# Performance work log

Hardware: AMD Instinct MI355X
Metric: run time of the kernel (lower is better)

## Reference

```python
import jax, jax.numpy as jnp
import numpy as np

B, N, C, H = 2, 2048, 1024, 16
D = C // H  # head_dim = 64


def setup_inputs() -> dict:
    key = jax.random.key(0)
    k1, k2, k3, k4 = jax.random.split(key, 4)
    x = jax.random.normal(k1, (B, N, C), dtype=jnp.float32)
    # params (torch Linear: y = x @ W.T + b). Store as [in, out] for einsum.
    w_qkv = jax.random.normal(k2, (C, 3 * C), dtype=jnp.float32) * (1.0 / np.sqrt(C))
    w_out = jax.random.normal(k3, (C, C), dtype=jnp.float32) * (1.0 / np.sqrt(C))
    b_out = jax.random.normal(k4, (C,), dtype=jnp.float32) * 0.01
    # causal mask: 1 above the diagonal -> masked_fill(-inf)
    attn_mask = jnp.triu(jnp.ones((N, N), dtype=jnp.int32), k=1)
    return {"x": x, "w_qkv": w_qkv, "w_out": w_out, "b_out": b_out, "attn_mask": attn_mask}


def reference(x, w_qkv, w_out, b_out, attn_mask):
    b, n, c = x.shape
    scale = 1.0 / jnp.sqrt(jnp.asarray(D, dtype=x.dtype))
    qkv = jnp.einsum('bnc,cd->bnd', x, w_qkv)                # [B, N, 3C]
    qkv = qkv.reshape(b, n, 3, H, D)
    q = qkv[:, :, 0].transpose(0, 2, 1, 3)                   # [B, H, N, D]
    k = qkv[:, :, 1].transpose(0, 2, 1, 3)
    v = qkv[:, :, 2].transpose(0, 2, 1, 3)
    scores = jnp.einsum('bhqd,bhkd->bhqk', q, k) * scale     # [B, H, N, N]
    scores = jnp.where(attn_mask == 1, jnp.asarray(-jnp.inf, dtype=scores.dtype), scores)
    attn = jax.nn.softmax(scores, axis=-1)
    # dropout is identity in eval mode (deterministic reference)
    out = jnp.einsum('bhqk,bhkd->bhqd', attn, v)             # [B, H, N, D]
    out = out.transpose(0, 2, 1, 3).reshape(b, n, c)         # [B, N, C]
    return jnp.einsum('bnc,cd->bnd', out, w_out) + b_out
```

## Files before the change

### kernel.cpp

```cpp
#include <hip/hip_runtime.h>

typedef _Float16 f16;
typedef _Float16 f16x8 __attribute__((ext_vector_type(8)));
typedef _Float16 f16x4 __attribute__((ext_vector_type(4)));
typedef float    f32x4 __attribute__((ext_vector_type(4)));

#define MFMA16(a, b, c) __builtin_amdgcn_mfma_f32_16x16x32_f16((a), (b), (c), 0, 0, 0)

__device__ __forceinline__ void gload16(const void* g, void* l) {
  __builtin_amdgcn_global_load_lds(
      (const __attribute__((address_space(1))) unsigned int*)g,
      (__attribute__((address_space(3))) unsigned int*)l, 16, 0, 0);
}

__device__ __forceinline__ float ex2(float x) {
  float r;
  asm("v_exp_f32 %0, %1" : "=v"(r) : "v"(x));
  return r;
}


__global__ void cast_f32_f16(const float* __restrict__ in, f16* __restrict__ out, int n4) {
  int i = blockIdx.x * blockDim.x + threadIdx.x;
  if (i < n4) {
    float4 v = ((const float4*)in)[i];
    f16x4 o;
    o.x = (f16)v.x; o.y = (f16)v.y; o.z = (f16)v.z; o.w = (f16)v.w;
    ((f16x4*)out)[i] = o;
  }
}

__global__ void transpose_cast(const float* __restrict__ in, f16* __restrict__ out, int R, int Cc) {
  __shared__ float tile[32][33];
  int c0 = blockIdx.x * 32, r0 = blockIdx.y * 32;
  int tx = threadIdx.x, ty = threadIdx.y;
#pragma unroll
  for (int i = ty; i < 32; i += 8)
    tile[i][tx] = in[(size_t)(r0 + i) * Cc + c0 + tx];
  __syncthreads();
#pragma unroll
  for (int i = ty; i < 32; i += 8)
    out[(size_t)(c0 + i) * R + r0 + tx] = (f16)tile[tx][i];
}

template <int KDIM>
__device__ __forceinline__ void gemm_core(const f16* __restrict__ A, const f16* __restrict__ Bt,
                                          int bm, int bn, f16* lA, f16* lB, f32x4 acc[4][4]) {
  const int t = threadIdx.x, lane = t & 63, wave = t >> 6;
  const int wm = wave >> 1, wn = wave & 1;
  const int srow = lane >> 3;
  const int skb = (lane & 7) * 16;
  const int nkt = KDIM / 64;
  for (int kt = 0; kt < nkt; ++kt) {
    __syncthreads();
#pragma unroll
    for (int c = 0; c < 4; ++c) {
      int cc = c * 4 + wave;
      int row = cc * 8 + srow;
      int kbs = skb ^ ((row & 7) << 4);
      gload16((const char*)A + (size_t)(bm * 128 + row) * (KDIM * 2) + kt * 128 + kbs,
              lA + cc * 512);
      gload16((const char*)Bt + (size_t)(bn * 128 + row) * (KDIM * 2) + kt * 128 + kbs,
              lB + cc * 512);
    }
    __syncthreads();
#pragma unroll
    for (int ks = 0; ks < 2; ++ks) {
      f16x8 af[4], bf[4];
#pragma unroll
      for (int mi = 0; mi < 4; ++mi) {
        int r = wm * 64 + mi * 16 + (lane & 15);
        int ke = (ks * 32 + ((lane >> 4) << 3)) ^ ((r & 7) << 3);
        af[mi] = *(const f16x8*)&lA[r * 64 + ke];
      }
#pragma unroll
      for (int ni = 0; ni < 4; ++ni) {
        int r = wn * 64 + ni * 16 + (lane & 15);
        int ke = (ks * 32 + ((lane >> 4) << 3)) ^ ((r & 7) << 3);
        bf[ni] = *(const f16x8*)&lB[r * 64 + ke];
      }
#pragma unroll
      for (int mi = 0; mi < 4; ++mi)
#pragma unroll
        for (int ni = 0; ni < 4; ++ni)
          acc[mi][ni] = MFMA16(af[mi], bf[ni], acc[mi][ni]);
    }
  }
}

__global__ __launch_bounds__(256, 2) void gemm_qkv(const f16* __restrict__ A,
                                                   const f16* __restrict__ Bt,
                                                   f16* __restrict__ Qo, f16* __restrict__ Ko,
                                                   f16* __restrict__ Vt) {
  __shared__ __align__(16) f16 lA[128 * 64];
  __shared__ __align__(16) f16 lB[128 * 64];
  f32x4 acc[4][4] = {};
  int w = blockIdx.x;
  int xcd = w & 7, i = w >> 3;
  int xr = xcd >> 1, xc = xcd & 1;
  int bm = xr * 8 + (i & 7);
  int bn = xc * 12 + (i >> 3);
  gemm_core<1024>(A, Bt, bm, bn, lA, lB, acc);
  int lane = threadIdx.x & 63, wave = threadIdx.x >> 6;
  int wm = wave >> 1, wn = wave & 1;
  int sec = (bn * 128) >> 10;
  float scl = (sec == 0) ? 0.18033688f : 1.0f;
#pragma unroll
  for (int mi = 0; mi < 4; ++mi)
#pragma unroll
    for (int ni = 0; ni < 4; ++ni)
#pragma unroll
      for (int reg = 0; reg < 4; ++reg) {
        int gr = bm * 128 + wm * 64 + mi * 16 + ((lane >> 4) << 2) + reg;
        int gc = bn * 128 + wn * 64 + ni * 16 + (lane & 15);
        int b = gr >> 11, n = gr & 2047;
        int jj = gc & 1023;
        int h = jj >> 6, d = jj & 63;
        f16 v = (f16)(acc[mi][ni][reg] * scl);
        size_t bh = (size_t)(b * 16 + h);
        if (sec == 0)      Qo[(bh * 2048 + n) * 64 + d] = v;
        else if (sec == 1) Ko[(bh * 2048 + n) * 64 + d] = v;
        else {
          int np = (n & ~31) | (((n >> 2) & 3) << 3) | (((n >> 4) & 1) << 2) | (n & 3);
          Vt[(bh * 64 + d) * 2048 + np] = v;
        }
      }
}

__device__ __forceinline__ void attn_one(const f16* __restrict__ Qb, const f16* __restrict__ Kb,
                                         const f16* __restrict__ Vb, f16* __restrict__ Ob,
                                         int qt, int lane, int wave, f16* lK, f16* lV) {
  const int N = 2048;
  const int wq0 = qt * 64 + wave * 16;
  const int g = lane >> 4, q15 = lane & 15;
  f16x8 qf[2];
#pragma unroll
  for (int ks = 0; ks < 2; ++ks)
    qf[ks] = *(const f16x8*)&Qb[(size_t)(wq0 + q15) * 64 + ks * 32 + (g << 3)];
  f32x4 oacc[4] = {};
  float mrun = -1e30f, lrun = 0.f;
  const int srow = lane >> 3, skb = (lane & 7) * 16;
  const int ntiles = qt + 1;

  auto STAGE = [&](int buf, int kv) {
    int kv0 = kv << 6;
#pragma unroll
    for (int c = 0; c < 2; ++c) {
      int cc = c * 4 + wave;
      int row = cc * 8 + srow;
      int kbs = skb ^ ((row & 7) << 4);
      gload16((const char*)Kb + (size_t)(kv0 + row) * 128 + kbs, lK + buf * 4096 + cc * 512);
      gload16((const char*)Vb + (size_t)row * (N * 2) + (size_t)kv0 * 2 + kbs,
              lV + buf * 4096 + cc * 512);
    }
  };

  STAGE(0, 0);
  __syncthreads();
  for (int kv = 0; kv < ntiles; ++kv) {
    int cur = kv & 1;
    if (kv + 1 < ntiles) STAGE(cur ^ 1, kv + 1);
    const f16* K0 = lK + cur * 4096;
    const f16* V0 = lV + cur * 4096;
    int kv0 = kv << 6;
    f32x4 s[4] = {};
    __builtin_amdgcn_s_setprio(1);
#pragma unroll
    for (int ks = 0; ks < 2; ++ks) {
      f16x8 kf[4];
#pragma unroll
      for (int ni = 0; ni < 4; ++ni) {
        int r = ni * 16 + q15;
        int ke = (ks * 32 + (g << 3)) ^ ((r & 7) << 3);
        kf[ni] = *(const f16x8*)&K0[r * 64 + ke];
      }
#pragma unroll
      for (int ni = 0; ni < 4; ++ni) s[ni] = MFMA16(kf[ni], qf[ks], s[ni]);
    }
    __builtin_amdgcn_s_setprio(0);
    if (kv == qt) {
      int gq = wq0 + q15;
#pragma unroll
      for (int ni = 0; ni < 4; ++ni)
#pragma unroll
        for (int reg = 0; reg < 4; ++reg) {
          int gk = kv0 + ni * 16 + g * 4 + reg;
          if (gk > gq) s[ni][reg] = -1e30f;
        }
    }
    f32x4 m4 = s[0];
#pragma unroll
    for (int ni = 1; ni < 4; ++ni)
#pragma unroll
      for (int reg = 0; reg < 4; ++reg) m4[reg] = fmaxf(m4[reg], s[ni][reg]);
    float mx = fmaxf(fmaxf(m4[0], m4[1]), fmaxf(m4[2], m4[3]));
    mx = fmaxf(mx, __shfl_xor(mx, 16));
    mx = fmaxf(mx, __shfl_xor(mx, 32));
    if (__any(mx > mrun)) {
      float mnew = fmaxf(mrun, mx);
      float corr = ex2(mrun - mnew);
      mrun = mnew;
      lrun *= corr;
#pragma unroll
      for (int ni = 0; ni < 4; ++ni)
#pragma unroll
        for (int reg = 0; reg < 4; ++reg) oacc[ni][reg] *= corr;
    }
    float rsum = 0.f;
#pragma unroll
    for (int ni = 0; ni < 4; ++ni)
#pragma unroll
      for (int reg = 0; reg < 4; ++reg) {
        float p = ex2(s[ni][reg] - mrun);
        s[ni][reg] = p;
        rsum += p;
      }
    rsum += __shfl_xor(rsum, 16);
    rsum += __shfl_xor(rsum, 32);
    lrun += rsum;
    f16x8 pf[2];
#pragma unroll
    for (int ks = 0; ks < 2; ++ks)
#pragma unroll
      for (int e = 0; e < 8; ++e) pf[ks][e] = (f16)s[2 * ks + (e >> 2)][e & 3];
    __builtin_amdgcn_s_setprio(1);
#pragma unroll
    for (int ks = 0; ks < 2; ++ks) {
      f16x8 vf[4];
#pragma unroll
      for (int mi = 0; mi < 4; ++mi) {
        int r = mi * 16 + q15;
        int ke = (ks * 32 + (g << 3)) ^ ((r & 7) << 3);
        vf[mi] = *(const f16x8*)&V0[r * 64 + ke];
      }
#pragma unroll
      for (int mi = 0; mi < 4; ++mi) oacc[mi] = MFMA16(vf[mi], pf[ks], oacc[mi]);
    }
    __builtin_amdgcn_s_setprio(0);
    __syncthreads();
  }
  float inv = 1.0f / lrun;
  int gq = wq0 + q15;
#pragma unroll
  for (int mi = 0; mi < 4; ++mi) {
    f16x4 o4;
#pragma unroll
    for (int reg = 0; reg < 4; ++reg) o4[reg] = (f16)(oacc[mi][reg] * inv);
    *(f16x4*)&Ob[(size_t)gq * 1024 + mi * 16 + g * 4] = o4;
  }
}

__global__ __launch_bounds__(256, 2) void attn(const f16* __restrict__ Q,
                                               const f16* __restrict__ K,
                                               const f16* __restrict__ Vt,
                                               f16* __restrict__ O) {
  __shared__ __align__(16) f16 lK[2 * 4096];
  __shared__ __align__(16) f16 lV[2 * 4096];
  int w = blockIdx.x;
  int c = w & 7, j = w >> 3;
  int bh = c * 4 + (j >> 4);
  int x = j & 15;
  int b = bh >> 4, h = bh & 15;
  int lane = threadIdx.x & 63, wave = threadIdx.x >> 6;
  const f16* Qb = Q + (size_t)bh * 2048 * 64;
  const f16* Kb = K + (size_t)bh * 2048 * 64;
  const f16* Vb = Vt + (size_t)bh * 2048 * 64;
  f16* Ob = O + (size_t)b * 2048 * 1024 + h * 64;
  attn_one(Qb, Kb, Vb, Ob, 31 - x, lane, wave, lK, lV);
  attn_one(Qb, Kb, Vb, Ob, x, lane, wave, lK, lV);
}

__global__ __launch_bounds__(256, 2) void gemm_out(const f16* __restrict__ A,
                                                   const f16* __restrict__ Bt,
                                                   const float* __restrict__ bias,
                                                   float* __restrict__ out) {
  __shared__ __align__(16) f16 lA[128 * 64];
  __shared__ __align__(16) f16 lB[128 * 64];
  f32x4 acc[4][4] = {};
  int w = blockIdx.x;
  int xcd = w & 7, i = w >> 3;
  int bm = xcd * 4 + (i & 3);
  int bn = i >> 2;
  gemm_core<1024>(A, Bt, bm, bn, lA, lB, acc);
  int lane = threadIdx.x & 63, wave = threadIdx.x >> 6;
  int wm = wave >> 1, wn = wave & 1;
#pragma unroll
  for (int mi = 0; mi < 4; ++mi)
#pragma unroll
    for (int ni = 0; ni < 4; ++ni)
#pragma unroll
      for (int reg = 0; reg < 4; ++reg) {
        int gr = bm * 128 + wm * 64 + mi * 16 + ((lane >> 4) << 2) + reg;
        int gc = bn * 128 + wn * 64 + ni * 16 + (lane & 15);
        out[(size_t)gr * 1024 + gc] = acc[mi][ni][reg] + bias[gc];
      }
}

extern "C" void kernel_launch(void* const* d_in, const int* in_sizes, int n_in,
                              void* d_out, int out_size, void* d_ws, size_t ws_size,
                              hipStream_t stream) {
  const float* x     = (const float*)d_in[0];
  const float* w_qkv = (const float*)d_in[1];
  const float* w_out = (const float*)d_in[2];
  const float* b_out = (const float*)d_in[3];
  float* out = (float*)d_out;
  char* ws = (char*)d_ws;

  f16* xh    = (f16*)(ws);
  f16* wqkvT = (f16*)(ws + (8u << 20));
  f16* woutT = (f16*)(ws + (14u << 20));
  f16* Qs    = (f16*)(ws + (16u << 20));
  f16* Ks    = (f16*)(ws + (24u << 20));
  f16* Vts   = (f16*)(ws + (32u << 20));
  f16* Oa    = (f16*)(ws + (40u << 20));

  cast_f32_f16<<<4096, 256, 0, stream>>>(x, xh, 1048576);
  transpose_cast<<<dim3(96, 32), dim3(32, 8), 0, stream>>>(w_qkv, wqkvT, 1024, 3072);
  transpose_cast<<<dim3(32, 32), dim3(32, 8), 0, stream>>>(w_out, woutT, 1024, 1024);
  gemm_qkv<<<768, 256, 0, stream>>>(xh, wqkvT, Qs, Ks, Vts);
  attn<<<512, 256, 0, stream>>>(Qs, Ks, Vts, Oa);
  gemm_out<<<256, 256, 0, stream>>>(Oa, woutT, b_out, out);
}
```

Measured before the change: 118.2 us.

## Double-buffer GEMM LDS tiles and widen attention KV tiles to 128

The shared GEMM core now double-buffers its A/B LDS tiles, so the next k-tile's global-to-LDS load is issued while MFMAs run on the current one. It also raises wave priority around the MFMA block and drops one barrier per iteration. Attention now processes 128 keys per iteration instead of 64, halving the number of loop iterations, barriers and softmax rescale checks, with the causal mask applied on the last tile. The cost is twice the LDS per block in all kernels (64KB each) and more registers for scores in attention, which may lower occupancy. Attention also does more masked wasted work on the diagonal tile.

```diff
diff --git a/kernel.cpp b/kernel.cpp
--- a/kernel.cpp
+++ b/kernel.cpp
@@ -51,19 +51,28 @@
   const int srow = lane >> 3;
   const int skb = (lane & 7) * 16;
   const int nkt = KDIM / 64;
-  for (int kt = 0; kt < nkt; ++kt) {
-    __syncthreads();
+
+  auto STAGE = [&](int buf, int kt) {
 #pragma unroll
     for (int c = 0; c < 4; ++c) {
       int cc = c * 4 + wave;
       int row = cc * 8 + srow;
       int kbs = skb ^ ((row & 7) << 4);
       gload16((const char*)A + (size_t)(bm * 128 + row) * (KDIM * 2) + kt * 128 + kbs,
-              lA + cc * 512);
+              lA + buf * 8192 + cc * 512);
       gload16((const char*)Bt + (size_t)(bn * 128 + row) * (KDIM * 2) + kt * 128 + kbs,
-              lB + cc * 512);
-    }
-    __syncthreads();
+              lB + buf * 8192 + cc * 512);
+    }
+  };
+
+  STAGE(0, 0);
+  __syncthreads();
+  for (int kt = 0; kt < nkt; ++kt) {
+    int cur = kt & 1;
+    if (kt + 1 < nkt) STAGE(cur ^ 1, kt + 1);
+    const f16* A0 = lA + cur * 8192;
+    const f16* B0 = lB + cur * 8192;
+    __builtin_amdgcn_s_setprio(1);
 #pragma unroll
     for (int ks = 0; ks < 2; ++ks) {
       f16x8 af[4], bf[4];
@@ -71,13 +80,13 @@
       for (int mi = 0; mi < 4; ++mi) {
         int r = wm * 64 + mi * 16 + (lane & 15);
         int ke = (ks * 32 + ((lane >> 4) << 3)) ^ ((r & 7) << 3);
-        af[mi] = *(const f16x8*)&lA[r * 64 + ke];
+        af[mi] = *(const f16x8*)&A0[r * 64 + ke];
       }
 #pragma unroll
       for (int ni = 0; ni < 4; ++ni) {
         int r = wn * 64 + ni * 16 + (lane & 15);
         int ke = (ks * 32 + ((lane >> 4) << 3)) ^ ((r & 7) << 3);
-        bf[ni] = *(const f16x8*)&lB[r * 64 + ke];
+        bf[ni] = *(const f16x8*)&B0[r * 64 + ke];
       }
 #pragma unroll
       for (int mi = 0; mi < 4; ++mi)
@@ -85,6 +94,8 @@
         for (int ni = 0; ni < 4; ++ni)
           acc[mi][ni] = MFMA16(af[mi], bf[ni], acc[mi][ni]);
     }
+    __builtin_amdgcn_s_setprio(0);
+    __syncthreads();
   }
 }
 
@@ -92,8 +103,8 @@
                                                    const f16* __restrict__ Bt,
                                                    f16* __restrict__ Qo, f16* __restrict__ Ko,
                                                    f16* __restrict__ Vt) {
-  __shared__ __align__(16) f16 lA[128 * 64];
-  __shared__ __align__(16) f16 lB[128 * 64];
+  __shared__ __align__(16) f16 lA[2 * 8192];
+  __shared__ __align__(16) f16 lB[2 * 8192];
   f32x4 acc[4][4] = {};
   int w = blockIdx.x;
   int xcd = w & 7, i = w >> 3;
@@ -140,18 +151,25 @@
   f32x4 oacc[4] = {};
   float mrun = -1e30f, lrun = 0.f;
   const int srow = lane >> 3, skb = (lane & 7) * 16;
-  const int ntiles = qt + 1;
+  const int ntiles = (qt >> 1) + 1;
 
   auto STAGE = [&](int buf, int kv) {
-    int kv0 = kv << 6;
-#pragma unroll
-    for (int c = 0; c < 2; ++c) {
+    int kv0 = kv << 7;
+#pragma unroll
+    for (int c = 0; c < 4; ++c) {
       int cc = c * 4 + wave;
-      int row = cc * 8 + srow;
-      int kbs = skb ^ ((row & 7) << 4);
-      gload16((const char*)Kb + (size_t)(kv0 + row) * 128 + kbs, lK + buf * 4096 + cc * 512);
-      gload16((const char*)Vb + (size_t)row * (N * 2) + (size_t)kv0 * 2 + kbs,
-              lV + buf * 4096 + cc * 512);
+      {
+        int row = cc * 8 + srow;
+        int kbs = skb ^ ((row & 7) << 4);
+        gload16((const char*)Kb + (size_t)(kv0 + row) * 128 + kbs, lK + buf * 8192 + cc * 512);
+      }
+      {
+        int sv = cc >> 3, c8 = cc & 7;
+        int row = c8 * 8 + srow;
+        int kbs = skb ^ ((row & 7) << 4);
+        gload16((const char*)Vb + (size_t)row * (N * 2) + (size_t)(kv0 + sv * 64) * 2 + kbs,
+                lV + buf * 8192 + sv * 4096 + c8 * 512);
+      }
     }
   };
 
@@ -160,28 +178,28 @@
   for (int kv = 0; kv < ntiles; ++kv) {
     int cur = kv & 1;
     if (kv + 1 < ntiles) STAGE(cur ^ 1, kv + 1);
-    const f16* K0 = lK + cur * 4096;
-    const f16* V0 = lV + cur * 4096;
-    int kv0 = kv << 6;
-    f32x4 s[4] = {};
+    const f16* K0 = lK + cur * 8192;
+    const f16* V0 = lV + cur * 8192;
+    int kv0 = kv << 7;
+    f32x4 s[8] = {};
     __builtin_amdgcn_s_setprio(1);
 #pragma unroll
     for (int ks = 0; ks < 2; ++ks) {
-      f16x8 kf[4];
-#pragma unroll
-      for (int ni = 0; ni < 4; ++ni) {
+      f16x8 kf[8];
+#pragma unroll
+      for (int ni = 0; ni < 8; ++ni) {
         int r = ni * 16 + q15;
         int ke = (ks * 32 + (g << 3)) ^ ((r & 7) << 3);
         kf[ni] = *(const f16x8*)&K0[r * 64 + ke];
       }
 #pragma unroll
-      for (int ni = 0; ni < 4; ++ni) s[ni] = MFMA16(kf[ni], qf[ks], s[ni]);
+      for (int ni = 0; ni < 8; ++ni) s[ni] = MFMA16(kf[ni], qf[ks], s[ni]);
     }
     __builtin_amdgcn_s_setprio(0);
-    if (kv == qt) {
+    if (kv == ntiles - 1) {
       int gq = wq0 + q15;
 #pragma unroll
-      for (int ni = 0; ni < 4; ++ni)
+      for (int ni = 0; ni < 8; ++ni)
 #pragma unroll
         for (int reg = 0; reg < 4; ++reg) {
           int gk = kv0 + ni * 16 + g * 4 + reg;
@@ -190,7 +208,7 @@
     }
     f32x4 m4 = s[0];
 #pragma unroll
-    for (int ni = 1; ni < 4; ++ni)
+    for (int ni = 1; ni < 8; ++ni)
 #pragma unroll
       for (int reg = 0; reg < 4; ++reg) m4[reg] = fmaxf(m4[reg], s[ni][reg]);
     float mx = fmaxf(fmaxf(m4[0], m4[1]), fmaxf(m4[2], m4[3]));
@@ -208,7 +226,7 @@
     }
     float rsum = 0.f;
 #pragma unroll
-    for (int ni = 0; ni < 4; ++ni)
+    for (int ni = 0; ni < 8; ++ni)
 #pragma unroll
       for (int reg = 0; reg < 4; ++reg) {
         float p = ex2(s[ni][reg] - mrun);
@@ -218,20 +236,21 @@
     rsum += __shfl_xor(rsum, 16);
     rsum += __shfl_xor(rsum, 32);
     lrun += rsum;
-    f16x8 pf[2];
-#pragma unroll
-    for (int ks = 0; ks < 2; ++ks)
+    f16x8 pf[4];
+#pragma unroll
+    for (int ks = 0; ks < 4; ++ks)
 #pragma unroll
       for (int e = 0; e < 8; ++e) pf[ks][e] = (f16)s[2 * ks + (e >> 2)][e & 3];
     __builtin_amdgcn_s_setprio(1);
 #pragma unroll
-    for (int ks = 0; ks < 2; ++ks) {
+    for (int ks = 0; ks < 4; ++ks) {
+      const f16* Vs = V0 + (ks >> 1) * 4096;
       f16x8 vf[4];
 #pragma unroll
       for (int mi = 0; mi < 4; ++mi) {
         int r = mi * 16 + q15;
-        int ke = (ks * 32 + (g << 3)) ^ ((r & 7) << 3);
-        vf[mi] = *(const f16x8*)&V0[r * 64 + ke];
+        int ke = ((ks & 1) * 32 + (g << 3)) ^ ((r & 7) << 3);
+        vf[mi] = *(const f16x8*)&Vs[r * 64 + ke];
       }
 #pragma unroll
       for (int mi = 0; mi < 4; ++mi) oacc[mi] = MFMA16(vf[mi], pf[ks], oacc[mi]);
@@ -254,8 +273,8 @@
                                                const f16* __restrict__ K,
                                                const f16* __restrict__ Vt,
                                                f16* __restrict__ O) {
-  __shared__ __align__(16) f16 lK[2 * 4096];
-  __shared__ __align__(16) f16 lV[2 * 4096];
+  __shared__ __align__(16) f16 lK[2 * 8192];
+  __shared__ __align__(16) f16 lV[2 * 8192];
   int w = blockIdx.x;
   int c = w & 7, j = w >> 3;
   int bh = c * 4 + (j >> 4);
@@ -274,8 +293,8 @@
                                                    const f16* __restrict__ Bt,
                                                    const float* __restrict__ bias,
                                                    float* __restrict__ out) {
-  __shared__ __align__(16) f16 lA[128 * 64];
-  __shared__ __align__(16) f16 lB[128 * 64];
+  __shared__ __align__(16) f16 lA[2 * 8192];
+  __shared__ __align__(16) f16 lB[2 * 8192];
   f32x4 acc[4][4] = {};
   int w = blockIdx.x;
   int xcd = w & 7, i = w >> 3;
```

Measured after the change: 119.4 us. Within noise of the previous version (+1.0%).
